# Kernel optimization log

Hardware: AMD Instinct MI355X
Metric: run time of the kernel (lower is better)

Reference implementation:

```python
import jax, jax.numpy as jnp
import numpy as np

IN_F = 4096
OUT_F = 4096
BATCH = 4
SEQ = 2048
QMAX = 16  # int4 levels


def setup_inputs() -> dict:
    key = jax.random.key(0)
    k_x, k_wq, k_s, k_z, k_t, k_m, k_b = jax.random.split(key, 7)
    x = jax.random.normal(k_x, (BATCH, SEQ, IN_F), dtype=jnp.float32)
    wq = jax.random.randint(k_wq, (OUT_F, IN_F), 0, QMAX, dtype=jnp.int32)
    qscale = jax.random.uniform(k_s, (OUT_F, 1), dtype=jnp.float32) * 0.01 + 1e-4
    qzero = jax.random.uniform(k_z, (OUT_F, 1), dtype=jnp.float32) * QMAX
    theta = jax.random.normal(k_t, (OUT_F, IN_F), dtype=jnp.float32) * 0.01
    mask = jax.random.randint(k_m, (OUT_F, IN_F), 0, 2, dtype=jnp.int32).astype(jnp.bool_)
    bias = jax.random.normal(k_b, (OUT_F,), dtype=jnp.float32) * 0.01
    return {"x": x, "wq": wq, "qscale": qscale, "qzero": qzero,
            "theta": theta, "mask": mask, "bias": bias}


def reference(x, wq, qscale, qzero, theta, mask, bias):
    # Per-output-channel int4 dequantization of active weights
    w_deq = (wq.astype(jnp.float32) - qzero) * qscale           # [out, in]
    m = mask.astype(jnp.float32)
    # Effective weight: active positions from dequantized W, pruned from theta
    w_eff = m * w_deq + (1.0 - m) * theta                        # [out, in]
    # F.linear: x @ W^T + b
    return jnp.einsum('bsi,oi->bso', x, w_eff) + bias
```

## Files before the change

### kernel.cpp

```cpp
#include <hip/hip_runtime.h>
#include <stdint.h>

typedef unsigned short u16;
typedef __bf16 bf16x8 __attribute__((ext_vector_type(8)));
typedef float f32x16 __attribute__((ext_vector_type(16)));

#define K_DIM 4096
#define N_OUT 4096
#define M_ROWS 8192


__device__ __forceinline__ u16 f2bf(float f) {
    uint32_t u = __builtin_bit_cast(uint32_t, f);
    u += 0x7fffu + ((u >> 16) & 1u);
    return (u16)(u >> 16);
}

__device__ __forceinline__ void gload_lds16(const void* g, void* l) {
    __builtin_amdgcn_global_load_lds(
        (const __attribute__((address_space(1))) void*)g,
        (__attribute__((address_space(3))) void*)l,
        16, 0, 0);
}

__device__ __forceinline__ int mask_is_int32(const void* maskp) {
    const uint32_t* u = (const uint32_t*)maskp;
    int ok = 1;
#pragma unroll
    for (int g = 0; g < 16; ++g) ok &= (u[g] <= 1u);
    return ok;
}


__global__ __launch_bounds__(256) void cvt_x_kernel(const float* __restrict__ x,
                                                    u16* __restrict__ xb) {
    size_t t = (size_t)blockIdx.x * 256 + threadIdx.x;
    const float4* p = (const float4*)x + t * 2;
    float4 a = p[0], b = p[1];
    union { u16 u[8]; uint4 v; } o;
    o.u[0] = f2bf(a.x); o.u[1] = f2bf(a.y); o.u[2] = f2bf(a.z); o.u[3] = f2bf(a.w);
    o.u[4] = f2bf(b.x); o.u[5] = f2bf(b.y); o.u[6] = f2bf(b.z); o.u[7] = f2bf(b.w);
    ((uint4*)xb)[t] = o.v;
}

__global__ __launch_bounds__(256) void build_w_kernel(const int* __restrict__ wq,
                                                      const float* __restrict__ qscale,
                                                      const float* __restrict__ qzero,
                                                      const float* __restrict__ theta,
                                                      const void* __restrict__ maskp,
                                                      u16* __restrict__ wb) {
    const int mi32 = mask_is_int32(maskp);
    size_t t = (size_t)blockIdx.x * 256 + threadIdx.x;
    size_t base = t * 8;
    int o = (int)(base >> 12);
    float s = qscale[o], z = qzero[o];

    int4 q0 = ((const int4*)wq)[t * 2];
    int4 q1 = ((const int4*)wq)[t * 2 + 1];
    float4 th0 = ((const float4*)theta)[t * 2];
    float4 th1 = ((const float4*)theta)[t * 2 + 1];

    int mv[8];
    if (mi32) {
        int4 m0 = ((const int4*)maskp)[t * 2];
        int4 m1 = ((const int4*)maskp)[t * 2 + 1];
        mv[0] = m0.x; mv[1] = m0.y; mv[2] = m0.z; mv[3] = m0.w;
        mv[4] = m1.x; mv[5] = m1.y; mv[6] = m1.z; mv[7] = m1.w;
    } else {
        uint2 mm = ((const uint2*)maskp)[t];
#pragma unroll
        for (int j = 0; j < 4; ++j) mv[j] = (mm.x >> (8 * j)) & 0xff;
#pragma unroll
        for (int j = 0; j < 4; ++j) mv[4 + j] = (mm.y >> (8 * j)) & 0xff;
    }

    float w[8];
    w[0] = mv[0] ? ((float)q0.x - z) * s : th0.x;
    w[1] = mv[1] ? ((float)q0.y - z) * s : th0.y;
    w[2] = mv[2] ? ((float)q0.z - z) * s : th0.z;
    w[3] = mv[3] ? ((float)q0.w - z) * s : th0.w;
    w[4] = mv[4] ? ((float)q1.x - z) * s : th1.x;
    w[5] = mv[5] ? ((float)q1.y - z) * s : th1.y;
    w[6] = mv[6] ? ((float)q1.z - z) * s : th1.z;
    w[7] = mv[7] ? ((float)q1.w - z) * s : th1.w;

    union { u16 u[8]; uint4 v; } ob;
#pragma unroll
    for (int j = 0; j < 8; ++j) ob.u[j] = f2bf(w[j]);
    ((uint4*)wb)[t] = ob.v;
}


__global__ __launch_bounds__(512, 2) void gemm8_kernel(const u16* __restrict__ xb,
                                                       const u16* __restrict__ wb,
                                                       const float* __restrict__ bias,
                                                       float* __restrict__ out) {
    __shared__ u16 lds[65536];

    const int tid = threadIdx.x;
    const int lane = tid & 63, wave = tid >> 6;
    const int wm = wave >> 2, wn = wave & 3;
    const int n0 = blockIdx.x * 256;
    const int m0 = blockIdx.y * 256;

    const int aR = wm * 128 + (lane & 31);
    const int bR = wn * 64 + (lane & 31);
    const int rs0 = (((lane >> 5) ^ ((lane >> 1) & 3))) * 8;
    const int rs1 = rs0 ^ 16;

    const int ch0 = wave * 2, ch1 = ch0 + 1;
    const int sRow = lane >> 2;
    const int sK = (((lane & 3) ^ ((lane >> 3) & 3)) * 8);
    const u16* gA0 = xb + (size_t)(m0 + ch0 * 16 + sRow) * K_DIM + sK;
    const u16* gA1 = xb + (size_t)(m0 + ch1 * 16 + sRow) * K_DIM + sK;
    const u16* gB0 = wb + (size_t)(n0 + ch0 * 16 + sRow) * K_DIM + sK;
    const u16* gB1 = wb + (size_t)(n0 + ch1 * 16 + sRow) * K_DIM + sK;

    f32x16 acc[4][2];
#pragma unroll
    for (int m = 0; m < 4; ++m)
#pragma unroll
        for (int n = 0; n < 2; ++n) acc[m][n] = (f32x16)(0.f);

#define SA(BUF, KH, KT) { \
    const size_t kofs = (size_t)((KT) * 64 + (KH) * 32); \
    const int pl = ((BUF) * 2 + (KH)) * 8192; \
    gload_lds16(gA0 + kofs, &lds[pl + ch0 * 512]); \
    gload_lds16(gA1 + kofs, &lds[pl + ch1 * 512]); }
#define SB(BUF, KH, KT) { \
    const size_t kofs = (size_t)((KT) * 64 + (KH) * 32); \
    const int pl = 32768 + ((BUF) * 2 + (KH)) * 8192; \
    gload_lds16(gB0 + kofs, &lds[pl + ch0 * 512]); \
    gload_lds16(gB1 + kofs, &lds[pl + ch1 * 512]); }
#define DA(BUF, KS, MH) { \
    const int pa = ((BUF) * 2 + (KS)) * 8192 + (aR + (MH) * 64) * 32; \
    af0 = *(const bf16x8*)&lds[pa + rs0]; \
    af1 = *(const bf16x8*)&lds[pa + rs1]; \
    af2 = *(const bf16x8*)&lds[pa + 1024 + rs0]; \
    af3 = *(const bf16x8*)&lds[pa + 1024 + rs1]; }
#define DB(BUF, KS) { \
    const int pb = 32768 + ((BUF) * 2 + (KS)) * 8192 + bR * 32; \
    bf0 = *(const bf16x8*)&lds[pb + rs0]; \
    bf1 = *(const bf16x8*)&lds[pb + rs1]; \
    bf2 = *(const bf16x8*)&lds[pb + 1024 + rs0]; \
    bf3 = *(const bf16x8*)&lds[pb + 1024 + rs1]; }
#define MFMA8(MH) { \
    __builtin_amdgcn_s_setprio(1); \
    acc[2*(MH)+0][0] = __builtin_amdgcn_mfma_f32_32x32x16_bf16(af0, bf0, acc[2*(MH)+0][0], 0, 0, 0); \
    acc[2*(MH)+0][1] = __builtin_amdgcn_mfma_f32_32x32x16_bf16(af0, bf2, acc[2*(MH)+0][1], 0, 0, 0); \
    acc[2*(MH)+1][0] = __builtin_amdgcn_mfma_f32_32x32x16_bf16(af2, bf0, acc[2*(MH)+1][0], 0, 0, 0); \
    acc[2*(MH)+1][1] = __builtin_amdgcn_mfma_f32_32x32x16_bf16(af2, bf2, acc[2*(MH)+1][1], 0, 0, 0); \
    acc[2*(MH)+0][0] = __builtin_amdgcn_mfma_f32_32x32x16_bf16(af1, bf1, acc[2*(MH)+0][0], 0, 0, 0); \
    acc[2*(MH)+0][1] = __builtin_amdgcn_mfma_f32_32x32x16_bf16(af1, bf3, acc[2*(MH)+0][1], 0, 0, 0); \
    acc[2*(MH)+1][0] = __builtin_amdgcn_mfma_f32_32x32x16_bf16(af3, bf1, acc[2*(MH)+1][0], 0, 0, 0); \
    acc[2*(MH)+1][1] = __builtin_amdgcn_mfma_f32_32x32x16_bf16(af3, bf3, acc[2*(MH)+1][1], 0, 0, 0); \
    __builtin_amdgcn_s_setprio(0); }
#define BAR() __builtin_amdgcn_s_barrier()
#define SCHED0() __builtin_amdgcn_sched_barrier(0)
#define VMW4() asm volatile("s_waitcnt vmcnt(4)" ::: "memory")

    SA(0, 0, 0); SB(0, 0, 0);
    SA(0, 1, 0); SB(0, 1, 0);
    SA(1, 0, 1); SB(1, 0, 1);
    asm volatile("s_waitcnt vmcnt(0)" ::: "memory");
    BAR();

#pragma unroll 1
    for (int j = 0; j < K_DIM / 128; ++j) {
        const int t1 = 2 * j + 1;
        const int t2 = (2 * j + 2) & 63;
        const int t3 = (2 * j + 3) & 63;
        bf16x8 af0, af1, af2, af3, bf0, bf1, bf2, bf3;
        DB(0, 0); DA(0, 0, 0); SA(1, 1, t1);
        BAR(); MFMA8(0); SCHED0(); BAR();
        DA(0, 0, 1); SB(1, 1, t1);
        BAR(); MFMA8(1); SCHED0(); BAR();
        DB(0, 1); DA(0, 1, 0); SA(0, 0, t2);
        BAR(); MFMA8(0); SCHED0(); BAR();
        DA(0, 1, 1); SB(0, 0, t2);
        BAR(); MFMA8(1); VMW4(); SCHED0(); BAR();
        DB(1, 0); DA(1, 0, 0); SA(0, 1, t2);
        BAR(); MFMA8(0); SCHED0(); BAR();
        DA(1, 0, 1); SB(0, 1, t2);
        BAR(); MFMA8(1); SCHED0(); BAR();
        DB(1, 1); DA(1, 1, 0); SA(1, 0, t3);
        BAR(); MFMA8(0); SCHED0(); BAR();
        DA(1, 1, 1); SB(1, 0, t3);
        BAR(); MFMA8(1); VMW4(); SCHED0(); BAR();
    }

    asm volatile("s_waitcnt vmcnt(0)" ::: "memory");

    const int colB = n0 + wn * 64 + (lane & 31);
    const int rowB = m0 + wm * 128 + ((lane >> 5) << 2);
#pragma unroll
    for (int n = 0; n < 2; ++n) {
        const int col = colB + n * 32;
        const float bv = bias[col];
#pragma unroll
        for (int m = 0; m < 4; ++m) {
            const f32x16 v = acc[m][n];
            float* o = out + (size_t)(rowB + m * 32) * N_OUT + col;
#pragma unroll
            for (int rg = 0; rg < 4; ++rg)
#pragma unroll
                for (int rr = 0; rr < 4; ++rr)
                    o[(size_t)(rg * 8 + rr) * N_OUT] = v[rg * 4 + rr] + bv;
        }
    }
#undef SA
#undef SB
#undef DA
#undef DB
#undef MFMA8
#undef BAR
#undef SCHED0
#undef VMW4
}


__global__ __launch_bounds__(256) void fallback_kernel(const float* __restrict__ x,
                                                       const int* __restrict__ wq,
                                                       const float* __restrict__ qscale,
                                                       const float* __restrict__ qzero,
                                                       const float* __restrict__ theta,
                                                       const void* __restrict__ maskp,
                                                       const float* __restrict__ bias,
                                                       float* __restrict__ out) {
    __shared__ float xs[64][17];
    __shared__ float wsh[64][17];
    const int mi32 = mask_is_int32(maskp);
    const int n0 = blockIdx.x * 64, m0 = blockIdx.y * 64;
    const int t = threadIdx.x;
    const int tr = t >> 4, tc = t & 15;
    float acc[4][4] = {};

    for (int k0 = 0; k0 < K_DIM; k0 += 16) {
#pragma unroll
        for (int j = 0; j < 4; ++j) {
            int e = t * 4 + j;
            int r = e >> 4, c = e & 15;
            xs[r][c] = x[(size_t)(m0 + r) * K_DIM + k0 + c];
            int o = n0 + r;
            size_t idx = (size_t)o * K_DIM + k0 + c;
            float dq = ((float)wq[idx] - qzero[o]) * qscale[o];
            int mv = mi32 ? ((const int*)maskp)[idx] : ((const unsigned char*)maskp)[idx];
            wsh[r][c] = mv ? dq : theta[idx];
        }
        __syncthreads();
#pragma unroll
        for (int kk = 0; kk < 16; ++kk) {
            float a4[4], b4[4];
#pragma unroll
            for (int i = 0; i < 4; ++i) a4[i] = xs[tr * 4 + i][kk];
#pragma unroll
            for (int i = 0; i < 4; ++i) b4[i] = wsh[tc * 4 + i][kk];
#pragma unroll
            for (int i = 0; i < 4; ++i)
#pragma unroll
                for (int j = 0; j < 4; ++j) acc[i][j] += a4[i] * b4[j];
        }
        __syncthreads();
    }
#pragma unroll
    for (int i = 0; i < 4; ++i)
#pragma unroll
        for (int j = 0; j < 4; ++j)
            out[(size_t)(m0 + tr * 4 + i) * N_OUT + n0 + tc * 4 + j] =
                acc[i][j] + bias[n0 + tc * 4 + j];
}


extern "C" void kernel_launch(void* const* d_in, const int* in_sizes, int n_in,
                              void* d_out, int out_size, void* d_ws, size_t ws_size,
                              hipStream_t stream) {
    const float* x      = (const float*)d_in[0];
    const int*   wq     = (const int*)d_in[1];
    const float* qscale = (const float*)d_in[2];
    const float* qzero  = (const float*)d_in[3];
    const float* theta  = (const float*)d_in[4];
    const void*  mask   = d_in[5];
    const float* bias   = (const float*)d_in[6];
    float* out = (float*)d_out;

    const size_t xb_bytes = (size_t)M_ROWS * K_DIM * 2;
    const size_t wb_bytes = (size_t)N_OUT * K_DIM * 2;

    if (ws_size >= xb_bytes + wb_bytes) {
        u16* xb = (u16*)d_ws;
        u16* wb = (u16*)((char*)d_ws + xb_bytes);
        cvt_x_kernel<<<16384, 256, 0, stream>>>(x, xb);
        build_w_kernel<<<8192, 256, 0, stream>>>(wq, qscale, qzero, theta, mask, wb);
        dim3 grid(N_OUT / 256, M_ROWS / 256);
        gemm8_kernel<<<grid, 512, 0, stream>>>(xb, wb, bias, out);
    } else {
        dim3 grid(N_OUT / 64, M_ROWS / 64);
        fallback_kernel<<<grid, 256, 0, stream>>>(x, wq, qscale, qzero, theta, mask, bias, out);
    }
}
```

Before: 344.1 us.

## Merge prep kernels and double-buffer LDS fragment reads in GEMM main loop

Merges the x-to-bf16 conversion and the weight build into one launch that picks its role by block index, saving a kernel launch and its tail. The GEMM main loop drops the barrier pair around each MFMA group: fragments for the next step are read into a second register set while the current MFMAs run, with one barrier per step. The LDS tile layout and the global-to-LDS address mapping are changed to match a new per-lane read pattern with a different XOR swizzle. This costs more registers for two fragment sets and makes correctness depend on the new swizzle and the reduced synchronisation.

Measured after the change: 400.2 us. +16.3%, slower.

```diff
diff --git a/kernel.cpp b/kernel.cpp
--- a/kernel.cpp
+++ b/kernel.cpp
@@ -32,62 +32,63 @@
 }
 
 
-__global__ __launch_bounds__(256) void cvt_x_kernel(const float* __restrict__ x,
-                                                    u16* __restrict__ xb) {
-    size_t t = (size_t)blockIdx.x * 256 + threadIdx.x;
-    const float4* p = (const float4*)x + t * 2;
-    float4 a = p[0], b = p[1];
-    union { u16 u[8]; uint4 v; } o;
-    o.u[0] = f2bf(a.x); o.u[1] = f2bf(a.y); o.u[2] = f2bf(a.z); o.u[3] = f2bf(a.w);
-    o.u[4] = f2bf(b.x); o.u[5] = f2bf(b.y); o.u[6] = f2bf(b.z); o.u[7] = f2bf(b.w);
-    ((uint4*)xb)[t] = o.v;
-}
-
-__global__ __launch_bounds__(256) void build_w_kernel(const int* __restrict__ wq,
-                                                      const float* __restrict__ qscale,
-                                                      const float* __restrict__ qzero,
-                                                      const float* __restrict__ theta,
-                                                      const void* __restrict__ maskp,
-                                                      u16* __restrict__ wb) {
-    const int mi32 = mask_is_int32(maskp);
-    size_t t = (size_t)blockIdx.x * 256 + threadIdx.x;
-    size_t base = t * 8;
-    int o = (int)(base >> 12);
-    float s = qscale[o], z = qzero[o];
-
-    int4 q0 = ((const int4*)wq)[t * 2];
-    int4 q1 = ((const int4*)wq)[t * 2 + 1];
-    float4 th0 = ((const float4*)theta)[t * 2];
-    float4 th1 = ((const float4*)theta)[t * 2 + 1];
-
-    int mv[8];
-    if (mi32) {
-        int4 m0 = ((const int4*)maskp)[t * 2];
-        int4 m1 = ((const int4*)maskp)[t * 2 + 1];
-        mv[0] = m0.x; mv[1] = m0.y; mv[2] = m0.z; mv[3] = m0.w;
-        mv[4] = m1.x; mv[5] = m1.y; mv[6] = m1.z; mv[7] = m1.w;
+__global__ __launch_bounds__(256) void prep_kernel(const float* __restrict__ x,
+                                                   u16* __restrict__ xb,
+                                                   const int* __restrict__ wq,
+                                                   const float* __restrict__ qscale,
+                                                   const float* __restrict__ qzero,
+                                                   const float* __restrict__ theta,
+                                                   const void* __restrict__ maskp,
+                                                   u16* __restrict__ wb) {
+    if (blockIdx.x < 16384) {
+        size_t t = (size_t)blockIdx.x * 256 + threadIdx.x;
+        const float4* p = (const float4*)x + t * 2;
+        float4 a = p[0], b = p[1];
+        union { u16 u[8]; uint4 v; } o;
+        o.u[0] = f2bf(a.x); o.u[1] = f2bf(a.y); o.u[2] = f2bf(a.z); o.u[3] = f2bf(a.w);
+        o.u[4] = f2bf(b.x); o.u[5] = f2bf(b.y); o.u[6] = f2bf(b.z); o.u[7] = f2bf(b.w);
+        ((uint4*)xb)[t] = o.v;
     } else {
-        uint2 mm = ((const uint2*)maskp)[t];
-#pragma unroll
-        for (int j = 0; j < 4; ++j) mv[j] = (mm.x >> (8 * j)) & 0xff;
-#pragma unroll
-        for (int j = 0; j < 4; ++j) mv[4 + j] = (mm.y >> (8 * j)) & 0xff;
-    }
-
-    float w[8];
-    w[0] = mv[0] ? ((float)q0.x - z) * s : th0.x;
-    w[1] = mv[1] ? ((float)q0.y - z) * s : th0.y;
-    w[2] = mv[2] ? ((float)q0.z - z) * s : th0.z;
-    w[3] = mv[3] ? ((float)q0.w - z) * s : th0.w;
-    w[4] = mv[4] ? ((float)q1.x - z) * s : th1.x;
-    w[5] = mv[5] ? ((float)q1.y - z) * s : th1.y;
-    w[6] = mv[6] ? ((float)q1.z - z) * s : th1.z;
-    w[7] = mv[7] ? ((float)q1.w - z) * s : th1.w;
-
-    union { u16 u[8]; uint4 v; } ob;
-#pragma unroll
-    for (int j = 0; j < 8; ++j) ob.u[j] = f2bf(w[j]);
-    ((uint4*)wb)[t] = ob.v;
+        const int mi32 = mask_is_int32(maskp);
+        size_t t = (size_t)(blockIdx.x - 16384) * 256 + threadIdx.x;
+        size_t base = t * 8;
+        int o = (int)(base >> 12);
+        float s = qscale[o], z = qzero[o];
+
+        int4 q0 = ((const int4*)wq)[t * 2];
+        int4 q1 = ((const int4*)wq)[t * 2 + 1];
+        float4 th0 = ((const float4*)theta)[t * 2];
+        float4 th1 = ((const float4*)theta)[t * 2 + 1];
+
+        int mv[8];
+        if (mi32) {
+            int4 m0 = ((const int4*)maskp)[t * 2];
+            int4 m1 = ((const int4*)maskp)[t * 2 + 1];
+            mv[0] = m0.x; mv[1] = m0.y; mv[2] = m0.z; mv[3] = m0.w;
+            mv[4] = m1.x; mv[5] = m1.y; mv[6] = m1.z; mv[7] = m1.w;
+        } else {
+            uint2 mm = ((const uint2*)maskp)[t];
+#pragma unroll
+            for (int j = 0; j < 4; ++j) mv[j] = (mm.x >> (8 * j)) & 0xff;
+#pragma unroll
+            for (int j = 0; j < 4; ++j) mv[4 + j] = (mm.y >> (8 * j)) & 0xff;
+        }
+
+        float w[8];
+        w[0] = mv[0] ? ((float)q0.x - z) * s : th0.x;
+        w[1] = mv[1] ? ((float)q0.y - z) * s : th0.y;
+        w[2] = mv[2] ? ((float)q0.z - z) * s : th0.z;
+        w[3] = mv[3] ? ((float)q0.w - z) * s : th0.w;
+        w[4] = mv[4] ? ((float)q1.x - z) * s : th1.x;
+        w[5] = mv[5] ? ((float)q1.y - z) * s : th1.y;
+        w[6] = mv[6] ? ((float)q1.z - z) * s : th1.z;
+        w[7] = mv[7] ? ((float)q1.w - z) * s : th1.w;
+
+        union { u16 u[8]; uint4 v; } ob;
+#pragma unroll
+        for (int j = 0; j < 8; ++j) ob.u[j] = f2bf(w[j]);
+        ((uint4*)wb)[t] = ob.v;
+    }
 }
 
 
@@ -103,57 +104,59 @@
     const int n0 = blockIdx.x * 256;
     const int m0 = blockIdx.y * 256;
 
-    const int aR = wm * 128 + (lane & 31);
-    const int bR = wn * 64 + (lane & 31);
-    const int rs0 = (((lane >> 5) ^ ((lane >> 1) & 3))) * 8;
-    const int rs1 = rs0 ^ 16;
-
-    const int ch0 = wave * 2, ch1 = ch0 + 1;
-    const int sRow = lane >> 2;
-    const int sK = (((lane & 3) ^ ((lane >> 3) & 3)) * 8);
-    const u16* gA0 = xb + (size_t)(m0 + ch0 * 16 + sRow) * K_DIM + sK;
-    const u16* gA1 = xb + (size_t)(m0 + ch1 * 16 + sRow) * K_DIM + sK;
-    const u16* gB0 = wb + (size_t)(n0 + ch0 * 16 + sRow) * K_DIM + sK;
-    const u16* gB1 = wb + (size_t)(n0 + ch1 * 16 + sRow) * K_DIM + sK;
+    const int xr = (lane & 31) ^ ((lane >> 5) << 2);
+    const int aOff = (lane >> 5) * 2048 + (wm * 128 + xr) * 8;
+    const int bOff = 32768 + (lane >> 5) * 2048 + (wn * 64 + xr) * 8;
+
+    const int hS = (wave >> 1) & 1, tS = wave >> 2;
+    const int dst0 = (wave >> 1) * 2048 + (wave & 1) * 1024;
+    const int dst1 = dst0 + 512;
+    const int srow0 = (wave & 1) * 128 + (lane ^ (hS << 2));
+    const int srow1 = srow0 + 64;
+    const int scol = tS * 16 + hS * 8;
+    const u16* gA0 = xb + (size_t)(m0 + srow0) * K_DIM + scol;
+    const u16* gA1 = xb + (size_t)(m0 + srow1) * K_DIM + scol;
+    const u16* gB0 = wb + (size_t)(n0 + srow0) * K_DIM + scol;
+    const u16* gB1 = wb + (size_t)(n0 + srow1) * K_DIM + scol;
 
     f32x16 acc[4][2];
 #pragma unroll
     for (int m = 0; m < 4; ++m)
 #pragma unroll
         for (int n = 0; n < 2; ++n) acc[m][n] = (f32x16)(0.f);
+
+    bf16x8 afA0, afA1, afA2, afA3, bfA0, bfA1;
+    bf16x8 afB0, afB1, afB2, afB3, bfB0, bfB1;
 
 #define SA(BUF, KH, KT) { \
     const size_t kofs = (size_t)((KT) * 64 + (KH) * 32); \
     const int pl = ((BUF) * 2 + (KH)) * 8192; \
-    gload_lds16(gA0 + kofs, &lds[pl + ch0 * 512]); \
-    gload_lds16(gA1 + kofs, &lds[pl + ch1 * 512]); }
+    gload_lds16(gA0 + kofs, &lds[pl + dst0]); \
+    gload_lds16(gA1 + kofs, &lds[pl + dst1]); }
 #define SB(BUF, KH, KT) { \
     const size_t kofs = (size_t)((KT) * 64 + (KH) * 32); \
     const int pl = 32768 + ((BUF) * 2 + (KH)) * 8192; \
-    gload_lds16(gB0 + kofs, &lds[pl + ch0 * 512]); \
-    gload_lds16(gB1 + kofs, &lds[pl + ch1 * 512]); }
-#define DA(BUF, KS, MH) { \
-    const int pa = ((BUF) * 2 + (KS)) * 8192 + (aR + (MH) * 64) * 32; \
-    af0 = *(const bf16x8*)&lds[pa + rs0]; \
-    af1 = *(const bf16x8*)&lds[pa + rs1]; \
-    af2 = *(const bf16x8*)&lds[pa + 1024 + rs0]; \
-    af3 = *(const bf16x8*)&lds[pa + 1024 + rs1]; }
-#define DB(BUF, KS) { \
-    const int pb = 32768 + ((BUF) * 2 + (KS)) * 8192 + bR * 32; \
-    bf0 = *(const bf16x8*)&lds[pb + rs0]; \
-    bf1 = *(const bf16x8*)&lds[pb + rs1]; \
-    bf2 = *(const bf16x8*)&lds[pb + 1024 + rs0]; \
-    bf3 = *(const bf16x8*)&lds[pb + 1024 + rs1]; }
-#define MFMA8(MH) { \
+    gload_lds16(gB0 + kofs, &lds[pl + dst0]); \
+    gload_lds16(gB1 + kofs, &lds[pl + dst1]); }
+#define RD(S, PL, T) { \
+    const int rb = (PL) * 8192 + (T) * 4096; \
+    af##S##0 = *(const bf16x8*)&lds[rb + aOff]; \
+    af##S##1 = *(const bf16x8*)&lds[rb + 256 + aOff]; \
+    af##S##2 = *(const bf16x8*)&lds[rb + 512 + aOff]; \
+    af##S##3 = *(const bf16x8*)&lds[rb + 768 + aOff]; \
+    bf##S##0 = *(const bf16x8*)&lds[rb + bOff]; \
+    bf##S##1 = *(const bf16x8*)&lds[rb + 256 + bOff]; }
+#define MF(A, B, C) __builtin_amdgcn_mfma_f32_32x32x16_bf16(A, B, C, 0, 0, 0)
+#define MFMA8(S) { \
     __builtin_amdgcn_s_setprio(1); \
-    acc[2*(MH)+0][0] = __builtin_amdgcn_mfma_f32_32x32x16_bf16(af0, bf0, acc[2*(MH)+0][0], 0, 0, 0); \
-    acc[2*(MH)+0][1] = __builtin_amdgcn_mfma_f32_32x32x16_bf16(af0, bf2, acc[2*(MH)+0][1], 0, 0, 0); \
-    acc[2*(MH)+1][0] = __builtin_amdgcn_mfma_f32_32x32x16_bf16(af2, bf0, acc[2*(MH)+1][0], 0, 0, 0); \
-    acc[2*(MH)+1][1] = __builtin_amdgcn_mfma_f32_32x32x16_bf16(af2, bf2, acc[2*(MH)+1][1], 0, 0, 0); \
-    acc[2*(MH)+0][0] = __builtin_amdgcn_mfma_f32_32x32x16_bf16(af1, bf1, acc[2*(MH)+0][0], 0, 0, 0); \
-    acc[2*(MH)+0][1] = __builtin_amdgcn_mfma_f32_32x32x16_bf16(af1, bf3, acc[2*(MH)+0][1], 0, 0, 0); \
-    acc[2*(MH)+1][0] = __builtin_amdgcn_mfma_f32_32x32x16_bf16(af3, bf1, acc[2*(MH)+1][0], 0, 0, 0); \
-    acc[2*(MH)+1][1] = __builtin_amdgcn_mfma_f32_32x32x16_bf16(af3, bf3, acc[2*(MH)+1][1], 0, 0, 0); \
+    acc[0][0] = MF(af##S##0, bf##S##0, acc[0][0]); \
+    acc[0][1] = MF(af##S##0, bf##S##1, acc[0][1]); \
+    acc[1][0] = MF(af##S##1, bf##S##0, acc[1][0]); \
+    acc[1][1] = MF(af##S##1, bf##S##1, acc[1][1]); \
+    acc[2][0] = MF(af##S##2, bf##S##0, acc[2][0]); \
+    acc[2][1] = MF(af##S##2, bf##S##1, acc[2][1]); \
+    acc[3][0] = MF(af##S##3, bf##S##0, acc[3][0]); \
+    acc[3][1] = MF(af##S##3, bf##S##1, acc[3][1]); \
     __builtin_amdgcn_s_setprio(0); }
 #define BAR() __builtin_amdgcn_s_barrier()
 #define SCHED0() __builtin_amdgcn_sched_barrier(0)
@@ -164,29 +167,37 @@
     SA(1, 0, 1); SB(1, 0, 1);
     asm volatile("s_waitcnt vmcnt(0)" ::: "memory");
     BAR();
+    RD(A, 0, 0);
 
 #pragma unroll 1
     for (int j = 0; j < K_DIM / 128; ++j) {
         const int t1 = 2 * j + 1;
         const int t2 = (2 * j + 2) & 63;
         const int t3 = (2 * j + 3) & 63;
-        bf16x8 af0, af1, af2, af3, bf0, bf1, bf2, bf3;
-        DB(0, 0); DA(0, 0, 0); SA(1, 1, t1);
-        BAR(); MFMA8(0); SCHED0(); BAR();
-        DA(0, 0, 1); SB(1, 1, t1);
-        BAR(); MFMA8(1); SCHED0(); BAR();
-        DB(0, 1); DA(0, 1, 0); SA(0, 0, t2);
-        BAR(); MFMA8(0); SCHED0(); BAR();
-        DA(0, 1, 1); SB(0, 0, t2);
-        BAR(); MFMA8(1); VMW4(); SCHED0(); BAR();
-        DB(1, 0); DA(1, 0, 0); SA(0, 1, t2);
-        BAR(); MFMA8(0); SCHED0(); BAR();
-        DA(1, 0, 1); SB(0, 1, t2);
-        BAR(); MFMA8(1); SCHED0(); BAR();
-        DB(1, 1); DA(1, 1, 0); SA(1, 0, t3);
-        BAR(); MFMA8(0); SCHED0(); BAR();
-        DA(1, 1, 1); SB(1, 0, t3);
-        BAR(); MFMA8(1); VMW4(); SCHED0(); BAR();
+        MFMA8(A); VMW4();
+        RD(B, 0, 1); SA(1, 1, t1);
+        SCHED0(); BAR();
+        MFMA8(B);
+        RD(A, 1, 0); SB(1, 1, t1);
+        SCHED0(); BAR();
+        MFMA8(A); VMW4();
+        RD(B, 1, 1); SA(0, 0, t2);
+        SCHED0(); BAR();
+        MFMA8(B);
+        RD(A, 2, 0); SB(0, 0, t2);
+        SCHED0(); BAR();
+        MFMA8(A); VMW4();
+        RD(B, 2, 1); SA(0, 1, t2);
+        SCHED0(); BAR();
+        MFMA8(B);
+        RD(A, 3, 0); SB(0, 1, t2);
+        SCHED0(); BAR();
+        MFMA8(A); VMW4();
+        RD(B, 3, 1); SA(1, 0, t3);
+        SCHED0(); BAR();
+        MFMA8(B);
+        RD(A, 0, 0); SB(1, 0, t3);
+        SCHED0(); BAR();
     }
 
     asm volatile("s_waitcnt vmcnt(0)" ::: "memory");
@@ -210,8 +221,8 @@
     }
 #undef SA
 #undef SB
-#undef DA
-#undef DB
+#undef RD
+#undef MF
 #undef MFMA8
 #undef BAR
 #undef SCHED0
@@ -289,8 +300,7 @@
     if (ws_size >= xb_bytes + wb_bytes) {
         u16* xb = (u16*)d_ws;
         u16* wb = (u16*)((char*)d_ws + xb_bytes);
-        cvt_x_kernel<<<16384, 256, 0, stream>>>(x, xb);
-        build_w_kernel<<<8192, 256, 0, stream>>>(wq, qscale, qzero, theta, mask, wb);
+        prep_kernel<<<24576, 256, 0, stream>>>(x, xb, wq, qscale, qzero, theta, mask, wb);
         dim3 grid(N_OUT / 256, M_ROWS / 256);
         gemm8_kernel<<<grid, 512, 0, stream>>>(xb, wb, bias, out);
     } else {
```
